# Kernel tuning notes

Hardware: AMD Instinct MI355X
Metric: run time of the kernel (lower is better)

## Reference

```python
import jax, jax.numpy as jnp
import numpy as np

N_NODES = 200000
N_EDGES = 1600000
N_GRAPHS = 2000
IN_DIM, W1_DIM, W2_DIM, N_CLASSES = 8, 64, 12, 2


def setup_inputs() -> dict:
    key = jax.random.key(0)
    ks = jax.random.split(key, 9)
    x = jax.random.normal(ks[0], (N_NODES, IN_DIM), dtype=jnp.float32)
    edge_index = jax.random.randint(ks[1], (2, N_EDGES), 0, N_NODES, dtype=jnp.int64)
    batch_index = jnp.sort(jax.random.randint(ks[2], (N_NODES,), 0, N_GRAPHS, dtype=jnp.int64))
    # Glorot-ish scaled params
    W1 = jax.random.normal(ks[3], (IN_DIM, W1_DIM), dtype=jnp.float32) * (1.0 / np.sqrt(IN_DIM))
    b1 = jnp.zeros((W1_DIM,), dtype=jnp.float32)
    W2 = jax.random.normal(ks[4], (W1_DIM, W2_DIM), dtype=jnp.float32) * (1.0 / np.sqrt(W1_DIM))
    b2 = jnp.zeros((W2_DIM,), dtype=jnp.float32)
    Wl = jax.random.normal(ks[5], (W2_DIM, N_CLASSES), dtype=jnp.float32) * (1.0 / np.sqrt(W2_DIM))
    bl = jnp.zeros((N_CLASSES,), dtype=jnp.float32)
    return {"x": x, "edge_index": edge_index, "batch_index": batch_index,
            "W1": W1, "b1": b1, "W2": W2, "b2": b2, "Wl": Wl, "bl": bl}


def _gcn_conv(x, W, b, src, dst, deg_inv_sqrt, n_nodes):
    # x' = D^{-1/2} (A + I) D^{-1/2} X W + b  (self-loops already in src/dst)
    xw = x @ W                                   # [N, out]
    norm = deg_inv_sqrt[src] * deg_inv_sqrt[dst]  # [E+N]
    msg = xw[src] * norm[:, None]                 # edge-wise gather (memory-bound)
    out = jax.ops.segment_sum(msg, dst, num_segments=n_nodes)
    return out + b


def reference(x, edge_index, batch_index, W1, b1, W2, b2, Wl, bl):
    n = x.shape[0]
    loops = jnp.arange(n, dtype=edge_index.dtype)
    src = jnp.concatenate([edge_index[0], loops])
    dst = jnp.concatenate([edge_index[1], loops])
    # degree (with self-loops) on destination nodes, as in PyG gcn_norm
    deg = jax.ops.segment_sum(jnp.ones_like(dst, dtype=x.dtype), dst, num_segments=n)
    deg_inv_sqrt = jax.lax.rsqrt(deg)  # deg >= 1 due to self-loops
    h = jax.nn.relu(_gcn_conv(x, W1, b1, src, dst, deg_inv_sqrt, n))
    h = jax.nn.relu(_gcn_conv(h, W2, b2, src, dst, deg_inv_sqrt, n))
    pooled = jax.ops.segment_max(h, batch_index, num_segments=N_GRAPHS)  # global_max_pool
    logits = pooled @ Wl + bl
    return jax.nn.log_softmax(logits, axis=1)
```

## Files before the change

### kernel.cpp

```cpp
#include <hip/hip_runtime.h>
#include <hip/hip_fp16.h>
#include <stdint.h>


constexpr int IN_DIM = 8;
constexpr int H1 = 64;
constexpr int H2 = 12;
constexpr int NPB = 256;
constexpr int NBK = 782;
constexpr int CAP = 2560;
constexpr int CHUNK = 4096;
constexpr int SLOTS = 16;

__device__ __forceinline__ void acc_row8(float* acc, int4 rv) {
    const __half2* h = (const __half2*)&rv;
#pragma unroll
    for (int q = 0; q < 4; ++q) {
        float2 f = __half22float2(h[q]);
        acc[2 * q] += f.x; acc[2 * q + 1] += f.y;
    }
}

__global__ void __launch_bounds__(256) k_binA(
        const int* __restrict__ src, const int* __restrict__ dst,
        uint32_t* __restrict__ pairs, int* __restrict__ bcursor, int ne) {
    __shared__ int s_cnt[NBK];
    __shared__ int s_start[NBK];
    __shared__ int s_gb[NBK];
    __shared__ int s_tmp[256];
    __shared__ uint32_t s_img[CHUNK];
    __shared__ uint16_t s_bkt[CHUNK];
    int t = threadIdx.x;
    for (int i = t; i < NBK; i += 256) s_cnt[i] = 0;
    __syncthreads();
    int e0 = blockIdx.x * CHUNK;
    int cntblk = min(CHUNK, ne - e0);
    int rec[16];
#pragma unroll
    for (int i = 0; i < 16; ++i) {
        int e = e0 + i * 256 + t;
        rec[i] = -1;
        if (e < ne) {
            int d = __builtin_nontemporal_load(&dst[e]);
            int b = d >> 8;
            int off = atomicAdd(&s_cnt[b], 1);
            rec[i] = (off << 18) | ((d & 255) << 10) | b;
        }
    }
    __syncthreads();
    int b4 = t * 4;
    int v0 = (b4 < NBK) ? s_cnt[b4] : 0;
    int v1 = (b4 + 1 < NBK) ? s_cnt[b4 + 1] : 0;
    int v2 = (b4 + 2 < NBK) ? s_cnt[b4 + 2] : 0;
    int v3 = (b4 + 3 < NBK) ? s_cnt[b4 + 3] : 0;
    int p1 = v0, p2 = v0 + v1, p3 = v0 + v1 + v2, tot = p3 + v3;
    s_tmp[t] = tot;
    __syncthreads();
    for (int off = 1; off < 256; off <<= 1) {
        int u = (t >= off) ? s_tmp[t - off] : 0;
        __syncthreads();
        s_tmp[t] += u;
        __syncthreads();
    }
    int ex = s_tmp[t] - tot;
    if (b4 < NBK)     s_start[b4] = ex;
    if (b4 + 1 < NBK) s_start[b4 + 1] = ex + p1;
    if (b4 + 2 < NBK) s_start[b4 + 2] = ex + p2;
    if (b4 + 3 < NBK) s_start[b4 + 3] = ex + p3;
    for (int b = t; b < NBK; b += 256) {
        int c = s_cnt[b];
        s_gb[b] = (c > 0) ? atomicAdd(&bcursor[b], c) : 0;
    }
    __syncthreads();
#pragma unroll
    for (int i = 0; i < 16; ++i) {
        if (rec[i] < 0) continue;
        int e = e0 + i * 256 + t;
        int b = rec[i] & 1023;
        int dl = (rec[i] >> 10) & 255;
        int off = rec[i] >> 18;
        int pos = s_start[b] + off;
        s_img[pos] = ((uint32_t)dl << 18) | (uint32_t)__builtin_nontemporal_load(&src[e]);
        s_bkt[pos] = (uint16_t)b;
    }
    __syncthreads();
    for (int i = t; i < cntblk; i += 256) {
        int b = s_bkt[i];
        int goff = s_gb[b] + (i - s_start[b]);
        if (goff < CAP) pairs[(size_t)b * CAP + goff] = s_img[i];
    }
}

__global__ void __launch_bounds__(256) k_binB(
        const uint32_t* __restrict__ pairs, const int* __restrict__ bcursor,
        const float* __restrict__ x, int* __restrict__ csr_pad,
        int* __restrict__ csr_ovf, unsigned int* __restrict__ meta,
        float* __restrict__ dis, __half2* __restrict__ xdh, int n) {
    __shared__ int s_hist[NPB];
    __shared__ int s_start[NPB];
    __shared__ int s_cur[NPB];
    __shared__ int s_tmp[256];
    __shared__ int s_pad[NPB * SLOTS];
    int b = blockIdx.x;
    int t = threadIdx.x;
    int cnt = min(bcursor[b], CAP);
    const uint32_t* pb = pairs + (size_t)b * CAP;
    s_hist[t] = 0; s_cur[t] = 0;
    for (int i = t; i < NPB * SLOTS; i += 256) s_pad[i] = n;
    __syncthreads();
    for (int i = t; i < cnt; i += 256)
        atomicAdd(&s_hist[__builtin_nontemporal_load(&pb[i]) >> 18], 1);
    __syncthreads();
    int v = s_hist[t];
    s_tmp[t] = v;
    __syncthreads();
    for (int off = 1; off < 256; off <<= 1) {
        int u = (t >= off) ? s_tmp[t - off] : 0;
        __syncthreads();
        s_tmp[t] += u;
        __syncthreads();
    }
    s_start[t] = s_tmp[t] - v;
    __syncthreads();
    int cb = b * CAP;
    int node = (b << 8) + t;
    if (node < n) {
        int deg = s_hist[t];
        meta[node] = ((unsigned int)deg << 21) | (unsigned int)(cb + s_start[t]);
        float di = rsqrtf((float)(deg + 1));
        dis[node] = di;
        const float4* xi = (const float4*)(x + (size_t)node * IN_DIM);
        float4 a = xi[0], c = xi[1];
        union { __half2 h[4]; int iv[4]; } u;
        u.h[0] = __float22half2_rn(make_float2(a.x * di, a.y * di));
        u.h[1] = __float22half2_rn(make_float2(a.z * di, a.w * di));
        u.h[2] = __float22half2_rn(make_float2(c.x * di, c.y * di));
        u.h[3] = __float22half2_rn(make_float2(c.z * di, c.w * di));
        ((int4*)xdh)[node] = make_int4(u.iv[0], u.iv[1], u.iv[2], u.iv[3]);
    } else if (node == n) {
        ((int4*)xdh)[n] = make_int4(0, 0, 0, 0);
    }
    __syncthreads();
    for (int i = t; i < cnt; i += 256) {
        uint32_t p = __builtin_nontemporal_load(&pb[i]);
        int dl = p >> 18;
        int sidx = (int)(p & 0x3FFFFu);
        int pos = atomicAdd(&s_cur[dl], 1);
        if (pos < SLOTS) s_pad[dl * SLOTS + pos] = sidx;
        else             csr_ovf[cb + s_start[dl] + pos] = sidx;
    }
    __syncthreads();
    for (int i = t; i < NPB * SLOTS / 4; i += 256) {
        int node2 = (b << 8) + (i >> 2);
        if (node2 < n)
            ((int4*)csr_pad)[(size_t)(b << 8) * 4 + i] = ((int4*)s_pad)[i];
    }
}

__global__ void __launch_bounds__(256) k_agg1f(
        const int* __restrict__ csr_pad, const int* __restrict__ csr_ovf,
        const unsigned int* __restrict__ meta, const __half2* __restrict__ xdh,
        const float* __restrict__ dis, const float* __restrict__ W1,
        const float* __restrict__ b1, const float* __restrict__ W2,
        __half2* __restrict__ y2h, int n) {
    __shared__ float sW1[IN_DIM * H1];
    __shared__ float sW2[H1 * H2];
    __shared__ float sb1[H1];
    for (int i = threadIdx.x; i < IN_DIM * H1; i += 256) sW1[i] = W1[i];
    for (int i = threadIdx.x; i < H1 * H2; i += 256) sW2[i] = W2[i];
    if (threadIdx.x < H1) sb1[threadIdx.x] = b1[threadIdx.x];
    __syncthreads();
    int node = blockIdx.x * 256 + threadIdx.x;
    if (node > n) return;
    int4* orow = (int4*)y2h + (size_t)node * 2;
    if (node == n) {
        orow[0] = make_int4(0, 0, 0, 0);
        orow[1] = make_int4(0, 0, 0, 0);
        return;
    }
    const int4* pr = (const int4*)(csr_pad + (size_t)node * SLOTS);
    int4 p0 = pr[0], p1 = pr[1], p2 = pr[2], p3 = pr[3];
    unsigned int m = meta[node];
    const int4* xt = (const int4*)xdh;

    float acc[8] = {0, 0, 0, 0, 0, 0, 0, 0};
    int idx[16] = {p0.x, p0.y, p0.z, p0.w, p1.x, p1.y, p1.z, p1.w,
                   p2.x, p2.y, p2.z, p2.w, p3.x, p3.y, p3.z, p3.w};
    acc_row8(acc, xt[node]);
#pragma unroll
    for (int i = 0; i < 16; ++i) acc_row8(acc, xt[(size_t)idx[i]]);
    int deg = m >> 21;
    if (deg > SLOTS) {
        int r0 = (int)(m & 0x1FFFFF);
        for (int r = SLOTS; r < deg; ++r) acc_row8(acc, xt[(size_t)csr_ovf[r0 + r]]);
    }
    float di = dis[node];
    float z[8];
#pragma unroll
    for (int k = 0; k < 8; ++k) z[k] = acc[k] * di;

    float y2[H2];
#pragma unroll
    for (int j = 0; j < H2; ++j) y2[j] = 0.f;
    for (int d = 0; d < H1; ++d) {
        float h = sb1[d];
#pragma unroll
        for (int k = 0; k < 8; ++k) h = fmaf(z[k], sW1[k * H1 + d], h);
        h = fmaxf(h, 0.f);
#pragma unroll
        for (int j = 0; j < H2; ++j) y2[j] = fmaf(h, sW2[d * H2 + j], y2[j]);
    }
    union { __half2 h2v[8]; int iv[8]; } u;
#pragma unroll
    for (int q = 0; q < 6; ++q)
        u.h2v[q] = __float22half2_rn(make_float2(y2[2 * q] * di, y2[2 * q + 1] * di));
    u.h2v[6] = __float22half2_rn(make_float2(0.f, 0.f));
    u.h2v[7] = u.h2v[6];
    orow[0] = make_int4(u.iv[0], u.iv[1], u.iv[2], u.iv[3]);
    orow[1] = make_int4(u.iv[4], u.iv[5], u.iv[6], u.iv[7]);
}

__global__ void __launch_bounds__(256) k_agg2(
        const int* __restrict__ csr_pad, const int* __restrict__ csr_ovf,
        const unsigned int* __restrict__ meta, const __half2* __restrict__ y2h,
        const float* __restrict__ dis, const float* __restrict__ b2,
        const int* __restrict__ batch, unsigned int* __restrict__ pooled, int n) {
    int node = blockIdx.x * 256 + threadIdx.x;
    int lane = threadIdx.x & 63;
    bool active = node < n;
    float v[12] = {0, 0, 0, 0, 0, 0, 0, 0, 0, 0, 0, 0};
    int gid = 0x7fffffff;
    if (active) {
        const int4* pr = (const int4*)(csr_pad + (size_t)node * SLOTS);
        int4 p0 = pr[0], p1 = pr[1], p2 = pr[2], p3 = pr[3];
        unsigned int m = meta[node];
        const int4* yt = (const int4*)y2h;
        float acc[12] = {0, 0, 0, 0, 0, 0, 0, 0, 0, 0, 0, 0};
        auto addrow = [&](int nb) {
            int4 ra = yt[(size_t)nb * 2];
            int4 rb = yt[(size_t)nb * 2 + 1];
            const __half2* ha = (const __half2*)&ra;
            const __half2* hb = (const __half2*)&rb;
#pragma unroll
            for (int q = 0; q < 4; ++q) {
                float2 f = __half22float2(ha[q]);
                acc[2 * q] += f.x; acc[2 * q + 1] += f.y;
            }
#pragma unroll
            for (int q = 0; q < 2; ++q) {
                float2 f = __half22float2(hb[q]);
                acc[8 + 2 * q] += f.x; acc[9 + 2 * q] += f.y;
            }
        };
        int idx[16] = {p0.x, p0.y, p0.z, p0.w, p1.x, p1.y, p1.z, p1.w,
                       p2.x, p2.y, p2.z, p2.w, p3.x, p3.y, p3.z, p3.w};
        addrow(node);
#pragma unroll
        for (int i = 0; i < 16; ++i) addrow(idx[i]);
        int deg = m >> 21;
        if (deg > SLOTS) {
            int r0 = (int)(m & 0x1FFFFF);
            for (int r = SLOTS; r < deg; ++r) addrow(csr_ovf[r0 + r]);
        }
        float di = dis[node];
#pragma unroll
        for (int q = 0; q < 12; ++q) v[q] = fmaxf(fmaf(acc[q], di, b2[q]), 0.f);
        gid = batch[node];
    }
#pragma unroll
    for (int off = 1; off < 64; off <<= 1) {
        int g2 = __shfl_up(gid, off, 64);
        bool merge = (lane >= off) && (g2 == gid);
#pragma unroll
        for (int q = 0; q < 12; ++q) {
            float tv = __shfl_up(v[q], off, 64);
            if (merge) v[q] = fmaxf(v[q], tv);
        }
    }
    int gnext = __shfl_down(gid, 1, 64);
    bool last = (lane == 63) || (gnext != gid);
    if (last && gid != 0x7fffffff) {
        unsigned int* pp = pooled + (size_t)gid * 12;
#pragma unroll
        for (int q = 0; q < 12; ++q) atomicMax(&pp[q], __float_as_uint(v[q]));
    }
}

__global__ void k_head(const unsigned int* __restrict__ pooled,
                       const float* __restrict__ Wl, const float* __restrict__ bl,
                       float* __restrict__ out, int g) {
    int i = blockIdx.x * 256 + threadIdx.x;
    if (i >= g) return;
    float l0 = bl[0], l1 = bl[1];
#pragma unroll
    for (int k = 0; k < H2; ++k) {
        float pv = __uint_as_float(pooled[(size_t)i * 12 + k]);
        l0 = fmaf(pv, Wl[k * 2 + 0], l0);
        l1 = fmaf(pv, Wl[k * 2 + 1], l1);
    }
    float m = fmaxf(l0, l1);
    float lse = m + logf(expf(l0 - m) + expf(l1 - m));
    out[i * 2 + 0] = l0 - lse;
    out[i * 2 + 1] = l1 - lse;
}

extern "C" void kernel_launch(void* const* d_in, const int* in_sizes, int n_in,
                              void* d_out, int out_size, void* d_ws, size_t ws_size,
                              hipStream_t stream) {
    const float* x   = (const float*)d_in[0];
    const int* ei    = (const int*)d_in[1];
    const int* batch = (const int*)d_in[2];
    const float* W1  = (const float*)d_in[3];
    const float* b1  = (const float*)d_in[4];
    const float* W2  = (const float*)d_in[5];
    const float* b2  = (const float*)d_in[6];
    const float* Wl  = (const float*)d_in[7];
    const float* bl  = (const float*)d_in[8];
    float* out = (float*)d_out;

    const int N = in_sizes[0] / IN_DIM;
    const int E = in_sizes[1] / 2;
    const int G = out_size / 2;
    const int* src = ei;
    const int* dst = ei + E;

    auto cdiv = [](long long a, int b) { return (int)((a + b - 1) / b); };

    char* wp = (char*)d_ws;
    auto carve = [&](size_t bytes) {
        char* p = wp;
        wp += (bytes + 63) & ~(size_t)63;
        return p;
    };
    int*          bcursor = (int*)carve(NBK * 4);
    unsigned int* pooled  = (unsigned int*)carve((size_t)G * H2 * 4);
    unsigned int* meta    = (unsigned int*)carve((size_t)N * 4);
    float*        dis     = (float*)carve((size_t)N * 4);
    __half2*      xdh     = (__half2*)carve((size_t)(N + 1) * 16);
    __half2*      y2h     = (__half2*)carve((size_t)(N + 1) * 32);
    uint32_t*     pairs   = (uint32_t*)carve((size_t)NBK * CAP * 4);
    int*          csr_pad = (int*)carve((size_t)N * SLOTS * 4);
    int*          csr_ovf = (int*)carve((size_t)NBK * CAP * 4);

    size_t zspan = (char*)(pooled + (size_t)G * H2) - (char*)bcursor;
    (void)hipMemsetAsync(bcursor, 0, zspan, stream);

    k_binA<<<cdiv(E, CHUNK), 256, 0, stream>>>(src, dst, pairs, bcursor, E);
    k_binB<<<NBK, 256, 0, stream>>>(pairs, bcursor, x, csr_pad, csr_ovf,
                                    meta, dis, xdh, N);

    k_agg1f<<<cdiv((long long)N + 1, 256), 256, 0, stream>>>(
        csr_pad, csr_ovf, meta, xdh, dis, W1, b1, W2, y2h, N);
    k_agg2<<<cdiv(N, 256), 256, 0, stream>>>(csr_pad, csr_ovf, meta, y2h, dis, b2,
                                             batch, pooled, N);
    k_head<<<cdiv(G, 256), 256, 0, stream>>>(pooled, Wl, bl, out, G);
}
```

Baseline: 176.1 us.

## Halve binning chunk, single-pass CSR fill, read MLP weights from global

The edge-binning kernel now processes 2048 edges per block instead of 4096, giving more blocks and fewer registers per thread. The CSR build kernel reads each bucket's pairs once into registers, and the histogram atomic's return value doubles as the slot offset, which removes the second global read pass and the second atomic. The fused layer-1 kernel drops its shared-memory staging of W1/W2/b1 and reads them straight from global memory, relying on uniform scalar or cached loads. This removes a barrier and LDS traffic, but global weight reads may cost more if they are not served as scalar loads.

```diff
diff --git a/kernel.cpp b/kernel.cpp
--- a/kernel.cpp
+++ b/kernel.cpp
@@ -9,7 +9,7 @@
 constexpr int NPB = 256;
 constexpr int NBK = 782;
 constexpr int CAP = 2560;
-constexpr int CHUNK = 4096;
+constexpr int CHUNK = 2048;
 constexpr int SLOTS = 16;
 
 __device__ __forceinline__ void acc_row8(float* acc, int4 rv) {
@@ -35,9 +35,9 @@
     __syncthreads();
     int e0 = blockIdx.x * CHUNK;
     int cntblk = min(CHUNK, ne - e0);
-    int rec[16];
-#pragma unroll
-    for (int i = 0; i < 16; ++i) {
+    int rec[8];
+#pragma unroll
+    for (int i = 0; i < 8; ++i) {
         int e = e0 + i * 256 + t;
         rec[i] = -1;
         if (e < ne) {
@@ -73,7 +73,7 @@
     }
     __syncthreads();
 #pragma unroll
-    for (int i = 0; i < 16; ++i) {
+    for (int i = 0; i < 8; ++i) {
         if (rec[i] < 0) continue;
         int e = e0 + i * 256 + t;
         int b = rec[i] & 1023;
@@ -98,18 +98,29 @@
         float* __restrict__ dis, __half2* __restrict__ xdh, int n) {
     __shared__ int s_hist[NPB];
     __shared__ int s_start[NPB];
-    __shared__ int s_cur[NPB];
     __shared__ int s_tmp[256];
     __shared__ int s_pad[NPB * SLOTS];
     int b = blockIdx.x;
     int t = threadIdx.x;
     int cnt = min(bcursor[b], CAP);
     const uint32_t* pb = pairs + (size_t)b * CAP;
-    s_hist[t] = 0; s_cur[t] = 0;
+    s_hist[t] = 0;
     for (int i = t; i < NPB * SLOTS; i += 256) s_pad[i] = n;
     __syncthreads();
-    for (int i = t; i < cnt; i += 256)
-        atomicAdd(&s_hist[__builtin_nontemporal_load(&pb[i]) >> 18], 1);
+    uint32_t rdl[10];
+    uint32_t rsx[10];
+#pragma unroll
+    for (int r = 0; r < 10; ++r) {
+        int i = t + r * 256;
+        rdl[r] = 0xFFFFFFFFu;
+        if (i < cnt) {
+            uint32_t p = __builtin_nontemporal_load(&pb[i]);
+            int dl = (int)(p >> 18);
+            int off = atomicAdd(&s_hist[dl], 1);
+            rdl[r] = ((uint32_t)off << 8) | (uint32_t)dl;
+            rsx[r] = p & 0x3FFFFu;
+        }
+    }
     __syncthreads();
     int v = s_hist[t];
     s_tmp[t] = v;
@@ -140,12 +151,12 @@
     } else if (node == n) {
         ((int4*)xdh)[n] = make_int4(0, 0, 0, 0);
     }
-    __syncthreads();
-    for (int i = t; i < cnt; i += 256) {
-        uint32_t p = __builtin_nontemporal_load(&pb[i]);
-        int dl = p >> 18;
-        int sidx = (int)(p & 0x3FFFFu);
-        int pos = atomicAdd(&s_cur[dl], 1);
+#pragma unroll
+    for (int r = 0; r < 10; ++r) {
+        if (rdl[r] == 0xFFFFFFFFu) continue;
+        int dl = (int)(rdl[r] & 255u);
+        int pos = (int)(rdl[r] >> 8);
+        int sidx = (int)rsx[r];
         if (pos < SLOTS) s_pad[dl * SLOTS + pos] = sidx;
         else             csr_ovf[cb + s_start[dl] + pos] = sidx;
     }
@@ -163,13 +174,6 @@
         const float* __restrict__ dis, const float* __restrict__ W1,
         const float* __restrict__ b1, const float* __restrict__ W2,
         __half2* __restrict__ y2h, int n) {
-    __shared__ float sW1[IN_DIM * H1];
-    __shared__ float sW2[H1 * H2];
-    __shared__ float sb1[H1];
-    for (int i = threadIdx.x; i < IN_DIM * H1; i += 256) sW1[i] = W1[i];
-    for (int i = threadIdx.x; i < H1 * H2; i += 256) sW2[i] = W2[i];
-    if (threadIdx.x < H1) sb1[threadIdx.x] = b1[threadIdx.x];
-    __syncthreads();
     int node = blockIdx.x * 256 + threadIdx.x;
     if (node > n) return;
     int4* orow = (int4*)y2h + (size_t)node * 2;
@@ -203,12 +207,12 @@
 #pragma unroll
     for (int j = 0; j < H2; ++j) y2[j] = 0.f;
     for (int d = 0; d < H1; ++d) {
-        float h = sb1[d];
-#pragma unroll
-        for (int k = 0; k < 8; ++k) h = fmaf(z[k], sW1[k * H1 + d], h);
+        float h = b1[d];
+#pragma unroll
+        for (int k = 0; k < 8; ++k) h = fmaf(z[k], W1[k * H1 + d], h);
         h = fmaxf(h, 0.f);
 #pragma unroll
-        for (int j = 0; j < H2; ++j) y2[j] = fmaf(h, sW2[d * H2 + j], y2[j]);
+        for (int j = 0; j < H2; ++j) y2[j] = fmaf(h, W2[d * H2 + j], y2[j]);
     }
     union { __half2 h2v[8]; int iv[8]; } u;
 #pragma unroll
```

After: 175.7 us. No clear change (-0.2%).
